# Kernel tuning notes

Hardware: AMD Instinct MI355X
Metric: run time of the kernel (lower is better)

The kernel has to match this reference:

```python
import jax, jax.numpy as jnp
import numpy as np
from jax import lax

B, T, D_IN, D_OUT = 1, 24000, 598, 3
UNITS = [100, 100, 100]
EPS = 0.001


def _lstm(x, W, U, b):
    # x: [B,T,D]; W: [D,4U]; U: [U,4U]; b: [4U]. Keras gate order i,f,g,o.
    units = U.shape[0]
    xW = jnp.einsum('btd,dk->btk', x, W) + b  # precompute input projections

    def step(carry, xw_t):
        h, c = carry
        z = xw_t + h @ U
        i, f, g, o = jnp.split(z, 4, axis=-1)
        c = jax.nn.sigmoid(f) * c + jax.nn.sigmoid(i) * jnp.tanh(g)
        h = jax.nn.sigmoid(o) * jnp.tanh(c)
        return (h, c), h

    h0 = jnp.zeros((x.shape[0], units), x.dtype)
    (_, _), hs = lax.scan(step, (h0, h0), jnp.swapaxes(xW, 0, 1))
    return jnp.swapaxes(hs, 0, 1)  # [B,T,U]


def _bn(x, gamma, beta, mean, var):
    # inference-mode batch norm over last axis
    return (x - mean) * lax.rsqrt(var + EPS) * gamma + beta


def setup_inputs() -> dict:
    key = jax.random.key(0)
    ks = jax.random.split(key, 16)
    out = {"x": jax.random.normal(ks[0], (B, T, D_IN), jnp.float32)}
    d_prev = D_IN
    ki = 1
    for l, u in enumerate(UNITS, start=1):
        out[f"W{l}"] = jax.random.normal(ks[ki], (d_prev, 4 * u), jnp.float32) * (2.0 / d_prev) ** 0.5; ki += 1
        out[f"U{l}"] = jax.random.normal(ks[ki], (u, 4 * u), jnp.float32) * (1.0 / u) ** 0.5; ki += 1
        out[f"b{l}"] = jnp.zeros((4 * u,), jnp.float32)
        out[f"g{l}"] = jnp.ones((u,), jnp.float32)
        out[f"be{l}"] = jnp.zeros((u,), jnp.float32)
        out[f"m{l}"] = jnp.zeros((u,), jnp.float32)
        out[f"v{l}"] = jnp.ones((u,), jnp.float32)
        d_prev = u
    out["Wd"] = jax.random.normal(ks[ki], (d_prev, D_OUT), jnp.float32) * (2.0 / d_prev) ** 0.5
    out["bd"] = jnp.zeros((D_OUT,), jnp.float32)
    return out


def reference(x, W1, U1, b1, g1, be1, m1, v1,
              W2, U2, b2, g2, be2, m2, v2,
              W3, U3, b3, g3, be3, m3, v3, Wd, bd):
    h = x
    params = [(W1, U1, b1, g1, be1, m1, v1),
              (W2, U2, b2, g2, be2, m2, v2),
              (W3, U3, b3, g3, be3, m3, v3)]
    for (W, U, b, g, be, m, v) in params:
        h = _lstm(h, W, U, b)
        h = _bn(h, g, be, m, v)
    return jax.nn.softmax(h @ Wd + bd, axis=-1)
```

## Files before the change

### kernel.cpp

```cpp
#include <hip/hip_runtime.h>

#define T_STEPS 24000
#define DIN 598
#define NU 100
#define NG 400
#define KHALF 52
#define KPAIR 26
#define KPAD 104
#define CHUNK 240
#define NCHUNK 100
#define RING 4
#define RN (RING * CHUNK)

typedef float v2f __attribute__((ext_vector_type(2)));
typedef float v4f __attribute__((ext_vector_type(4)));

#define BARRIER_LDS() asm volatile("s_waitcnt lgkmcnt(0)\n\ts_barrier" ::: "memory")

#define PIN_V2(x) asm volatile("" : "+v"(x))

__device__ __forceinline__ float dpp_add_x1(float x) {
    int y = __builtin_amdgcn_mov_dpp(__float_as_int(x), 0xB1, 0xF, 0xF, true);
    return x + __int_as_float(y);
}

__device__ __forceinline__ void wg_wait_ge(int* flag, int target) {
    if (threadIdx.x == 0) {
        while (__hip_atomic_load(flag, __ATOMIC_RELAXED, __HIP_MEMORY_SCOPE_AGENT) < target)
            __builtin_amdgcn_s_sleep(2);
    }
    __syncthreads();
    __builtin_amdgcn_fence(__ATOMIC_ACQUIRE, "agent");
}
__device__ __forceinline__ void wg_publish(int* a, int va, int* b, int vb) {
    __syncthreads();
    if (threadIdx.x == 0) {
        if (a) __hip_atomic_store(a, va, __ATOMIC_RELEASE, __HIP_MEMORY_SCOPE_AGENT);
        if (b) __hip_atomic_store(b, vb, __ATOMIC_RELEASE, __HIP_MEMORY_SCOPE_AGENT);
    }
}

__device__ __forceinline__ float sigmoid_(float x) {
    return 1.f / (1.f + __expf(-x));
}
__device__ __forceinline__ float tanh_(float x) {
    float e = __expf(2.f * x);
    return 1.f - 2.f / (e + 1.f);
}

__global__ __launch_bounds__(256) void gemm_bias_kernel(
    const float* __restrict__ A, const float* __restrict__ B,
    const float* __restrict__ bias, float* __restrict__ C,
    int M, int N, int K)
{
    __shared__ float As[16][65];
    __shared__ float Bs[16][65];
    const int tid = threadIdx.x;
    const int tx = tid & 15;
    const int ty = tid >> 4;
    const int bm = blockIdx.y * 64;
    const int bn = blockIdx.x * 64;
    float acc[4][4] = {};

    for (int k0 = 0; k0 < K; k0 += 16) {
        #pragma unroll
        for (int p = 0; p < 4; ++p) {
            int e = tid + p * 256;
            int r = e >> 4, cc = e & 15;
            int m = bm + r, k = k0 + cc;
            float v = (m < M && k < K) ? A[(long)m * K + k] : 0.f;
            As[cc][r] = v;
        }
        #pragma unroll
        for (int p = 0; p < 4; ++p) {
            int e = tid + p * 256;
            int r = e >> 6, cc = e & 63;
            int k = k0 + r, n = bn + cc;
            float v = (k < K && n < N) ? B[(long)k * N + n] : 0.f;
            Bs[r][cc] = v;
        }
        __syncthreads();
        #pragma unroll
        for (int kk = 0; kk < 16; ++kk) {
            float a[4], b[4];
            #pragma unroll
            for (int i = 0; i < 4; ++i) a[i] = As[kk][ty * 4 + i];
            #pragma unroll
            for (int j = 0; j < 4; ++j) b[j] = Bs[kk][tx * 4 + j];
            #pragma unroll
            for (int i = 0; i < 4; ++i)
                #pragma unroll
                for (int j = 0; j < 4; ++j)
                    acc[i][j] += a[i] * b[j];
        }
        __syncthreads();
    }
    #pragma unroll
    for (int i = 0; i < 4; ++i) {
        int m = bm + ty * 4 + i;
        if (m >= M) continue;
        #pragma unroll
        for (int j = 0; j < 4; ++j) {
            int n = bn + tx * 4 + j;
            if (n < N) {
                int pn = (n % 100) * 4 + (n / 100);
                C[(long)m * N + pn] = acc[i][j] + bias[n];
            }
        }
    }
}

__device__ void rec_role(
    const float* __restrict__ xz, int xz_ring,
    const float* __restrict__ U,
    float* __restrict__ hout, long h_stride, int h_ring,
    int* flag_up, int* done_self, int* done_down, int* flag_self,
    float* lds)
{
    float* hb0 = lds;
    float* hb1 = lds + KPAD;
    const int tid = threadIdx.x;
    const bool active = tid < 2 * NU;
    const int u = tid >> 1;
    const int s = tid & 1;

    v2f u0[KPAIR], u1[KPAIR], u2[KPAIR], u3[KPAIR];
    if (active) {
        const int k0 = KHALF * s;
        #pragma unroll
        for (int j = 0; j < KPAIR; ++j) {
            int k = k0 + 2 * j;
            float a0 = 0.f, b0 = 0.f, a1 = 0.f, b1 = 0.f,
                  a2 = 0.f, b2 = 0.f, a3 = 0.f, b3 = 0.f;
            if (k < NU) {
                a0 = U[(long)k * NG + u];          a1 = U[(long)k * NG + NU + u];
                a2 = U[(long)k * NG + 2 * NU + u]; a3 = U[(long)k * NG + 3 * NU + u];
            }
            if (k + 1 < NU) {
                b0 = U[(long)(k + 1) * NG + u];          b1 = U[(long)(k + 1) * NG + NU + u];
                b2 = U[(long)(k + 1) * NG + 2 * NU + u]; b3 = U[(long)(k + 1) * NG + 3 * NU + u];
            }
            u0[j] = (v2f){a0, b0}; u1[j] = (v2f){a1, b1};
            u2[j] = (v2f){a2, b2}; u3[j] = (v2f){a3, b3};
            PIN_V2(u0[j]); PIN_V2(u1[j]); PIN_V2(u2[j]); PIN_V2(u3[j]);
        }
    }
    if (tid < KPAD) { hb0[tid] = 0.f; hb1[tid] = 0.f; }
    float c_state = 0.f;
    float2 xwp0 = make_float2(0.f, 0.f), xwp1 = xwp0, xwp2 = xwp0, xwp3 = xwp0;
    float4 hbatch = make_float4(0.f, 0.f, 0.f, 0.f);

    const float* xz_lane = xz + 4 * u + 2 * s;
    float* hout_u = hout + (long)u * h_stride;
    int nxt  = 4 * NG;
    int hoff = 0;
    __syncthreads();

    auto step = [&](const float* hrd, float* hwr, int t) {
        if (active) {
            const v4f* h4 = (const v4f*)(hrd + KHALF * s);
            float2 xw_use = xwp0;
            xwp0 = xwp1; xwp1 = xwp2; xwp2 = xwp3;
            if (t + 4 < T_STEPS) {
                xwp3 = *(const float2*)(xz_lane + nxt);
            }
            nxt += NG;
            if (xz_ring && nxt == RN * NG) nxt = 0;
            v2f a0 = (v2f){0.f, 0.f}, a1 = (v2f){0.f, 0.f};
            v2f a2 = (v2f){0.f, 0.f}, a3 = (v2f){0.f, 0.f};
            #pragma unroll
            for (int q = 0; q < 13; ++q) {
                v4f hv = h4[q];
                v2f plo = hv.xy;
                v2f phi = hv.zw;
                a0 = __builtin_elementwise_fma(u0[2 * q],     plo, a0);
                a1 = __builtin_elementwise_fma(u1[2 * q],     plo, a1);
                a2 = __builtin_elementwise_fma(u2[2 * q],     plo, a2);
                a3 = __builtin_elementwise_fma(u3[2 * q],     plo, a3);
                a0 = __builtin_elementwise_fma(u0[2 * q + 1], phi, a0);
                a1 = __builtin_elementwise_fma(u1[2 * q + 1], phi, a1);
                a2 = __builtin_elementwise_fma(u2[2 * q + 1], phi, a2);
                a3 = __builtin_elementwise_fma(u3[2 * q + 1], phi, a3);
            }
            float ax = a0.x + a0.y;
            float ay = a1.x + a1.y;
            float az = a2.x + a2.y;
            float aw = a3.x + a3.y;
            if (s == 0) { ax += xw_use.x; ay += xw_use.y; }
            else        { az += xw_use.x; aw += xw_use.y; }
            ax = dpp_add_x1(ax);
            ay = dpp_add_x1(ay);
            az = dpp_add_x1(az);
            aw = dpp_add_x1(aw);
            float iv = sigmoid_(ax);
            float fv = sigmoid_(ay);
            float gv = tanh_(az);
            float ov = sigmoid_(aw);
            c_state = fv * c_state + iv * gv;
            float h = ov * tanh_(c_state);
            if (s == 0) {
                hwr[u] = h;
                int ph = t & 3;
                if      (ph == 0) hbatch.x = h;
                else if (ph == 1) hbatch.y = h;
                else if (ph == 2) hbatch.z = h;
                else {
                    hbatch.w = h;
                    *(float4*)(hout_u + hoff) = hbatch;
                    hoff += 4;
                    if (h_ring && hoff == RN) hoff = 0;
                }
            }
        }
        BARRIER_LDS();
    };

    for (int c = 0; c < NCHUNK; ++c) {
        if (flag_up) {
            int tgt = c + 2; if (tgt > NCHUNK) tgt = NCHUNK;
            wg_wait_ge(flag_up, tgt);
        }
        if (done_down && c >= RING) wg_wait_ge(done_down, c - RING + 1);
        if (c == 0 && active) {
            xwp0 = *(const float2*)(xz_lane);
            xwp1 = *(const float2*)(xz_lane + NG);
            xwp2 = *(const float2*)(xz_lane + 2 * NG);
            xwp3 = *(const float2*)(xz_lane + 3 * NG);
        }
        const int t0 = c * CHUNK;
        for (int tt = 0; tt < CHUNK; tt += 2) {
            step(hb0, hb1, t0 + tt);
            step(hb1, hb0, t0 + tt + 1);
        }
        wg_publish(done_self, c + 1, flag_self, c + 1);
    }
}

__device__ void proj_role(
    const float* __restrict__ hin,
    const float* __restrict__ W,
    const float* __restrict__ bias,
    const float* __restrict__ g, const float* __restrict__ be,
    const float* __restrict__ m, const float* __restrict__ v,
    float* __restrict__ xzout,
    int* flag_up, int* done_self, int* done_down, int* flag_self,
    float* lds)
{
    const int tid = threadIdx.x;
    const bool active = tid < 2 * NU;
    const int u = tid >> 1;
    const int s = tid & 1;

    v2f w0[KPAIR], w1[KPAIR], w2[KPAIR], w3[KPAIR];
    float bx = 0.f, by = 0.f;
    if (active) {
        const int k0 = KHALF * s;
        float pbx = 0.f, pby = 0.f, pbz = 0.f, pbw = 0.f;
        #pragma unroll
        for (int j = 0; j < KPAIR; ++j) {
            int k = k0 + 2 * j;
            float a0 = 0.f, b0 = 0.f, a1 = 0.f, b1 = 0.f,
                  a2 = 0.f, b2 = 0.f, a3 = 0.f, b3 = 0.f;
            if (k < NU) {
                float sc = g[k] * rsqrtf(v[k] + 1e-3f);
                float sh = be[k] - m[k] * sc;
                float q0 = W[(long)k * NG + u];
                float q1 = W[(long)k * NG + NU + u];
                float q2 = W[(long)k * NG + 2 * NU + u];
                float q3 = W[(long)k * NG + 3 * NU + u];
                a0 = sc * q0; a1 = sc * q1; a2 = sc * q2; a3 = sc * q3;
                pbx += sh * q0; pby += sh * q1; pbz += sh * q2; pbw += sh * q3;
            }
            if (k + 1 < NU) {
                int kk = k + 1;
                float sc = g[kk] * rsqrtf(v[kk] + 1e-3f);
                float sh = be[kk] - m[kk] * sc;
                float q0 = W[(long)kk * NG + u];
                float q1 = W[(long)kk * NG + NU + u];
                float q2 = W[(long)kk * NG + 2 * NU + u];
                float q3 = W[(long)kk * NG + 3 * NU + u];
                b0 = sc * q0; b1 = sc * q1; b2 = sc * q2; b3 = sc * q3;
                pbx += sh * q0; pby += sh * q1; pbz += sh * q2; pbw += sh * q3;
            }
            w0[j] = (v2f){a0, b0}; w1[j] = (v2f){a1, b1};
            w2[j] = (v2f){a2, b2}; w3[j] = (v2f){a3, b3};
            PIN_V2(w0[j]); PIN_V2(w1[j]); PIN_V2(w2[j]); PIN_V2(w3[j]);
        }
        pbx += __shfl_xor(pbx, 1); pby += __shfl_xor(pby, 1);
        pbz += __shfl_xor(pbz, 1); pbw += __shfl_xor(pbw, 1);
        if (s == 0) { bx = bias[u]          + pbx; by = bias[NU + u]     + pby; }
        else        { bx = bias[2 * NU + u] + pbz; by = bias[3 * NU + u] + pbw; }
    }

    for (int c = 0; c < NCHUNK; ++c) {
        wg_wait_ge(flag_up, c + 1);
        if (c >= RING) wg_wait_ge(done_down, c - RING + 1);
        {
            const int tbase = (c % RING) * CHUNK;
            for (int idx = tid; idx < KPAD * CHUNK; idx += 256) {
                int k = idx / CHUNK, r = idx - k * CHUNK;
                lds[r * KPAD + k] = (k < NU) ? hin[(long)k * RN + tbase + r] : 0.f;
            }
        }
        wg_publish(done_self, c + 1, (int*)0, 0);
        if (active) {
            float* ob = xzout + (size_t)(c % RING) * CHUNK * NG;
            for (int r = 0; r < CHUNK; ++r) {
                const v4f* h4 = (const v4f*)(lds + r * KPAD + KHALF * s);
                v2f a0 = (v2f){0.f, 0.f}, a1 = (v2f){0.f, 0.f};
                v2f a2 = (v2f){0.f, 0.f}, a3 = (v2f){0.f, 0.f};
                #pragma unroll
                for (int q = 0; q < 13; ++q) {
                    v4f hv = h4[q];
                    v2f plo = hv.xy;
                    v2f phi = hv.zw;
                    a0 = __builtin_elementwise_fma(w0[2 * q],     plo, a0);
                    a1 = __builtin_elementwise_fma(w1[2 * q],     plo, a1);
                    a2 = __builtin_elementwise_fma(w2[2 * q],     plo, a2);
                    a3 = __builtin_elementwise_fma(w3[2 * q],     plo, a3);
                    a0 = __builtin_elementwise_fma(w0[2 * q + 1], phi, a0);
                    a1 = __builtin_elementwise_fma(w1[2 * q + 1], phi, a1);
                    a2 = __builtin_elementwise_fma(w2[2 * q + 1], phi, a2);
                    a3 = __builtin_elementwise_fma(w3[2 * q + 1], phi, a3);
                }
                float ax = a0.x + a0.y;
                float ay = a1.x + a1.y;
                float az = a2.x + a2.y;
                float aw = a3.x + a3.y;
                ax = dpp_add_x1(ax);
                ay = dpp_add_x1(ay);
                az = dpp_add_x1(az);
                aw = dpp_add_x1(aw);
                float2 o2 = (s == 0) ? make_float2(ax + bx, ay + by)
                                     : make_float2(az + bx, aw + by);
                *(float2*)&ob[(long)r * NG + 4 * u + 2 * s] = o2;
            }
        }
        wg_publish(flag_self, c + 1, (int*)0, 0);
    }
}

__global__ __launch_bounds__(256)
__attribute__((amdgpu_waves_per_eu(1, 1)))
void lstm_pipe_kernel(
    const float* xw1, const float* U1,
    const float* U2, const float* W2, const float* b2,
    const float* U3, const float* W3, const float* b3,
    const float* g1, const float* be1, const float* m1, const float* v1,
    const float* g2, const float* be2, const float* m2, const float* v2,
    float* h1r, float* h2r, float* xz2r, float* xz3r, float* h3,
    int* f)
{
    extern __shared__ float smem[];
    int* f_h1  = f +   0;
    int* d_p2  = f +  32;
    int* f_xz2 = f +  64;
    int* d_r2  = f +  96;
    int* f_h2  = f + 128;
    int* d_p3  = f + 160;
    int* f_xz3 = f + 192;
    int* d_r3  = f + 224;

    switch (blockIdx.x) {
    case 0: rec_role(xw1, 0, U1, h1r, RN, 1, (int*)0, (int*)0, d_p2, f_h1, smem); break;
    case 1: proj_role(h1r, W2, b2, g1, be1, m1, v1, xz2r, f_h1, d_p2, d_r2, f_xz2, smem); break;
    case 2: rec_role(xz2r, 1, U2, h2r, RN, 1, f_xz2, d_r2, d_p3, f_h2, smem); break;
    case 3: proj_role(h2r, W3, b3, g2, be2, m2, v2, xz3r, f_h2, d_p3, d_r3, f_xz3, smem); break;
    case 4: rec_role(xz3r, 1, U3, h3, T_STEPS, 0, f_xz3, d_r3, (int*)0, (int*)0, smem); break;
    }
}

__global__ __launch_bounds__(256) void dense_softmax_kernel(
    const float* __restrict__ H,
    const float* __restrict__ Wd,
    const float* __restrict__ bd,
    const float* __restrict__ g3, const float* __restrict__ be3,
    const float* __restrict__ m3, const float* __restrict__ v3,
    float* __restrict__ out, int T)
{
    __shared__ float w[300];
    __shared__ float b[3];
    const int tid = threadIdx.x;
    for (int i = tid; i < 300; i += 256) {
        int k = i / 3;
        float sc = g3[k] * rsqrtf(v3[k] + 1e-3f);
        w[i] = Wd[i] * sc;
    }
    if (tid < 3) {
        float acc = bd[tid];
        for (int k = 0; k < NU; ++k) {
            float sc = g3[k] * rsqrtf(v3[k] + 1e-3f);
            float sh = be3[k] - m3[k] * sc;
            acc += sh * Wd[3 * k + tid];
        }
        b[tid] = acc;
    }
    __syncthreads();

    int row = blockIdx.x * blockDim.x + tid;
    if (row >= T) return;
    float s0 = b[0], s1 = b[1], s2 = b[2];
    #pragma unroll 4
    for (int k = 0; k < NU; ++k) {
        float hv = H[(long)k * T + row];
        s0 += hv * w[3 * k + 0];
        s1 += hv * w[3 * k + 1];
        s2 += hv * w[3 * k + 2];
    }
    float mx = fmaxf(s0, fmaxf(s1, s2));
    float e0 = __expf(s0 - mx), e1 = __expf(s1 - mx), e2 = __expf(s2 - mx);
    float inv = 1.f / (e0 + e1 + e2);
    out[(long)row * 3 + 0] = e0 * inv;
    out[(long)row * 3 + 1] = e1 * inv;
    out[(long)row * 3 + 2] = e2 * inv;
}

extern "C" void kernel_launch(void* const* d_in, const int* in_sizes, int n_in,
                              void* d_out, int out_size, void* d_ws, size_t ws_size,
                              hipStream_t stream)
{
    const float* x   = (const float*)d_in[0];
    const float* W1  = (const float*)d_in[1];
    const float* U1  = (const float*)d_in[2];
    const float* b1  = (const float*)d_in[3];
    const float* ga1 = (const float*)d_in[4];
    const float* be1 = (const float*)d_in[5];
    const float* mu1 = (const float*)d_in[6];
    const float* va1 = (const float*)d_in[7];
    const float* W2  = (const float*)d_in[8];
    const float* U2  = (const float*)d_in[9];
    const float* b2  = (const float*)d_in[10];
    const float* ga2 = (const float*)d_in[11];
    const float* be2 = (const float*)d_in[12];
    const float* mu2 = (const float*)d_in[13];
    const float* va2 = (const float*)d_in[14];
    const float* W3  = (const float*)d_in[15];
    const float* U3  = (const float*)d_in[16];
    const float* b3  = (const float*)d_in[17];
    const float* ga3 = (const float*)d_in[18];
    const float* be3 = (const float*)d_in[19];
    const float* mu3 = (const float*)d_in[20];
    const float* va3 = (const float*)d_in[21];
    const float* Wd  = (const float*)d_in[22];
    const float* bd  = (const float*)d_in[23];

    float* xw1  = (float*)d_ws;
    float* h3   = xw1  + (size_t)T_STEPS * NG;
    float* h1r  = h3   + (size_t)T_STEPS * NU;
    float* h2r  = h1r  + (size_t)RN * NU;
    float* xz2r = h2r  + (size_t)RN * NU;
    float* xz3r = xz2r + (size_t)RN * NG;
    int*   flags = (int*)(xz3r + (size_t)RN * NG);
    float* out = (float*)d_out;

    dim3 blk(256);
    dim3 grd((NG + 63) / 64, (T_STEPS + 63) / 64);

    gemm_bias_kernel<<<grd, blk, 0, stream>>>(x, W1, b1, xw1, T_STEPS, NG, DIN);
    hipMemsetAsync(flags, 0, 512 * sizeof(int), stream);
    lstm_pipe_kernel<<<5, 256, CHUNK * KPAD * sizeof(float), stream>>>(
        xw1, U1, U2, W2, b2, U3, W3, b3,
        ga1, be1, mu1, va1, ga2, be2, mu2, va2,
        h1r, h2r, xz2r, xz3r, h3, flags);
    dense_softmax_kernel<<<(T_STEPS + 255) / 256, 256, 0, stream>>>(
        h3, Wd, bd, ga3, be3, mu3, va3, out, T_STEPS);
}
```

Before: 21.07 ms.

## Split LSTM gate work across four lanes per unit with 512-thread blocks

After: 20.43 ms. 1.03x faster.

```diff
diff --git a/kernel.cpp b/kernel.cpp
--- a/kernel.cpp
+++ b/kernel.cpp
@@ -11,6 +11,7 @@
 #define NCHUNK 100
 #define RING 4
 #define RN (RING * CHUNK)
+#define BLK 512
 
 typedef float v2f __attribute__((ext_vector_type(2)));
 typedef float v4f __attribute__((ext_vector_type(4)));
@@ -22,6 +23,10 @@
 __device__ __forceinline__ float dpp_add_x1(float x) {
     int y = __builtin_amdgcn_mov_dpp(__float_as_int(x), 0xB1, 0xF, 0xF, true);
     return x + __int_as_float(y);
+}
+__device__ __forceinline__ float dpp_get_x2(float x) {
+    int y = __builtin_amdgcn_mov_dpp(__float_as_int(x), 0x4E, 0xF, 0xF, true);
+    return __int_as_float(y);
 }
 
 __device__ __forceinline__ void wg_wait_ge(int* flag, int target) {
@@ -120,29 +125,24 @@
     float* hb0 = lds;
     float* hb1 = lds + KPAD;
     const int tid = threadIdx.x;
-    const bool active = tid < 2 * NU;
-    const int u = tid >> 1;
-    const int s = tid & 1;
-
-    v2f u0[KPAIR], u1[KPAIR], u2[KPAIR], u3[KPAIR];
+    const bool active = tid < 4 * NU;
+    const int u  = tid >> 2;
+    const int gp = (tid >> 1) & 1;
+    const int s  = tid & 1;
+
+    v2f wa[KPAIR], wb[KPAIR];
     if (active) {
         const int k0 = KHALF * s;
+        const int ga = 2 * gp * NU, gb = (2 * gp + 1) * NU;
         #pragma unroll
         for (int j = 0; j < KPAIR; ++j) {
             int k = k0 + 2 * j;
-            float a0 = 0.f, b0 = 0.f, a1 = 0.f, b1 = 0.f,
-                  a2 = 0.f, b2 = 0.f, a3 = 0.f, b3 = 0.f;
-            if (k < NU) {
-                a0 = U[(long)k * NG + u];          a1 = U[(long)k * NG + NU + u];
-                a2 = U[(long)k * NG + 2 * NU + u]; a3 = U[(long)k * NG + 3 * NU + u];
-            }
-            if (k + 1 < NU) {
-                b0 = U[(long)(k + 1) * NG + u];          b1 = U[(long)(k + 1) * NG + NU + u];
-                b2 = U[(long)(k + 1) * NG + 2 * NU + u]; b3 = U[(long)(k + 1) * NG + 3 * NU + u];
-            }
-            u0[j] = (v2f){a0, b0}; u1[j] = (v2f){a1, b1};
-            u2[j] = (v2f){a2, b2}; u3[j] = (v2f){a3, b3};
-            PIN_V2(u0[j]); PIN_V2(u1[j]); PIN_V2(u2[j]); PIN_V2(u3[j]);
+            float a0 = 0.f, a1 = 0.f, b0 = 0.f, b1 = 0.f;
+            if (k < NU)     { a0 = U[(long)k * NG + ga + u];       b0 = U[(long)k * NG + gb + u]; }
+            if (k + 1 < NU) { a1 = U[(long)(k + 1) * NG + ga + u]; b1 = U[(long)(k + 1) * NG + gb + u]; }
+            wa[j] = (v2f){a0, a1};
+            wb[j] = (v2f){b0, b1};
+            PIN_V2(wa[j]); PIN_V2(wb[j]);
         }
     }
     if (tid < KPAD) { hb0[tid] = 0.f; hb1[tid] = 0.f; }
@@ -150,7 +150,7 @@
     float2 xwp0 = make_float2(0.f, 0.f), xwp1 = xwp0, xwp2 = xwp0, xwp3 = xwp0;
     float4 hbatch = make_float4(0.f, 0.f, 0.f, 0.f);
 
-    const float* xz_lane = xz + 4 * u + 2 * s;
+    const float* xz_lane = xz + 4 * u + 2 * gp;
     float* hout_u = hout + (long)u * h_stride;
     int nxt  = 4 * NG;
     int hoff = 0;
@@ -159,6 +159,10 @@
     auto step = [&](const float* hrd, float* hwr, int t) {
         if (active) {
             const v4f* h4 = (const v4f*)(hrd + KHALF * s);
+            v4f hbuf[13];
+            #pragma unroll
+            for (int q = 0; q < 13; ++q) hbuf[q] = h4[q];
+            __builtin_amdgcn_sched_barrier(0);
             float2 xw_use = xwp0;
             xwp0 = xwp1; xwp1 = xwp2; xwp2 = xwp3;
             if (t + 4 < T_STEPS) {
@@ -166,39 +170,35 @@
             }
             nxt += NG;
             if (xz_ring && nxt == RN * NG) nxt = 0;
+            __builtin_amdgcn_sched_barrier(0);
             v2f a0 = (v2f){0.f, 0.f}, a1 = (v2f){0.f, 0.f};
-            v2f a2 = (v2f){0.f, 0.f}, a3 = (v2f){0.f, 0.f};
             #pragma unroll
             for (int q = 0; q < 13; ++q) {
-                v4f hv = h4[q];
-                v2f plo = hv.xy;
-                v2f phi = hv.zw;
-                a0 = __builtin_elementwise_fma(u0[2 * q],     plo, a0);
-                a1 = __builtin_elementwise_fma(u1[2 * q],     plo, a1);
-                a2 = __builtin_elementwise_fma(u2[2 * q],     plo, a2);
-                a3 = __builtin_elementwise_fma(u3[2 * q],     plo, a3);
-                a0 = __builtin_elementwise_fma(u0[2 * q + 1], phi, a0);
-                a1 = __builtin_elementwise_fma(u1[2 * q + 1], phi, a1);
-                a2 = __builtin_elementwise_fma(u2[2 * q + 1], phi, a2);
-                a3 = __builtin_elementwise_fma(u3[2 * q + 1], phi, a3);
+                v2f plo = hbuf[q].xy;
+                v2f phi = hbuf[q].zw;
+                a0 = __builtin_elementwise_fma(wa[2 * q],     plo, a0);
+                a1 = __builtin_elementwise_fma(wb[2 * q],     plo, a1);
+                a0 = __builtin_elementwise_fma(wa[2 * q + 1], phi, a0);
+                a1 = __builtin_elementwise_fma(wb[2 * q + 1], phi, a1);
             }
             float ax = a0.x + a0.y;
             float ay = a1.x + a1.y;
-            float az = a2.x + a2.y;
-            float aw = a3.x + a3.y;
-            if (s == 0) { ax += xw_use.x; ay += xw_use.y; }
-            else        { az += xw_use.x; aw += xw_use.y; }
+            if (s == gp) { ax += xw_use.x; ay += xw_use.y; }
             ax = dpp_add_x1(ax);
             ay = dpp_add_x1(ay);
-            az = dpp_add_x1(az);
-            aw = dpp_add_x1(aw);
-            float iv = sigmoid_(ax);
-            float fv = sigmoid_(ay);
-            float gv = tanh_(az);
-            float ov = sigmoid_(aw);
+            float bx2 = dpp_get_x2(ax);
+            float by2 = dpp_get_x2(ay);
+            float zi = gp ? bx2 : ax;
+            float zf = gp ? by2 : ay;
+            float zg = gp ? ax : bx2;
+            float zo = gp ? ay : by2;
+            float iv = sigmoid_(zi);
+            float fv = sigmoid_(zf);
+            float gv = tanh_(zg);
+            float ov = sigmoid_(zo);
             c_state = fv * c_state + iv * gv;
             float h = ov * tanh_(c_state);
-            if (s == 0) {
+            if ((tid & 3) == 0) {
                 hwr[u] = h;
                 int ph = t & 3;
                 if      (ph == 0) hbatch.x = h;
@@ -247,49 +247,45 @@
     float* lds)
 {
     const int tid = threadIdx.x;
-    const bool active = tid < 2 * NU;
-    const int u = tid >> 1;
-    const int s = tid & 1;
-
-    v2f w0[KPAIR], w1[KPAIR], w2[KPAIR], w3[KPAIR];
+    const bool active = tid < 4 * NU;
+    const int u  = tid >> 2;
+    const int gp = (tid >> 1) & 1;
+    const int s  = tid & 1;
+
+    v2f wa[KPAIR], wb[KPAIR];
     float bx = 0.f, by = 0.f;
     if (active) {
         const int k0 = KHALF * s;
-        float pbx = 0.f, pby = 0.f, pbz = 0.f, pbw = 0.f;
+        const int ga = 2 * gp * NU, gb = (2 * gp + 1) * NU;
+        float pba = 0.f, pbb = 0.f;
         #pragma unroll
         for (int j = 0; j < KPAIR; ++j) {
             int k = k0 + 2 * j;
-            float a0 = 0.f, b0 = 0.f, a1 = 0.f, b1 = 0.f,
-                  a2 = 0.f, b2 = 0.f, a3 = 0.f, b3 = 0.f;
+            float a0 = 0.f, a1 = 0.f, b0 = 0.f, b1 = 0.f;
             if (k < NU) {
                 float sc = g[k] * rsqrtf(v[k] + 1e-3f);
                 float sh = be[k] - m[k] * sc;
-                float q0 = W[(long)k * NG + u];
-                float q1 = W[(long)k * NG + NU + u];
-                float q2 = W[(long)k * NG + 2 * NU + u];
-                float q3 = W[(long)k * NG + 3 * NU + u];
-                a0 = sc * q0; a1 = sc * q1; a2 = sc * q2; a3 = sc * q3;
-                pbx += sh * q0; pby += sh * q1; pbz += sh * q2; pbw += sh * q3;
+                float qa = W[(long)k * NG + ga + u];
+                float qb = W[(long)k * NG + gb + u];
+                a0 = sc * qa; b0 = sc * qb;
+                pba += sh * qa; pbb += sh * qb;
             }
             if (k + 1 < NU) {
                 int kk = k + 1;
                 float sc = g[kk] * rsqrtf(v[kk] + 1e-3f);
                 float sh = be[kk] - m[kk] * sc;
-                float q0 = W[(long)kk * NG + u];
-                float q1 = W[(long)kk * NG + NU + u];
-                float q2 = W[(long)kk * NG + 2 * NU + u];
-                float q3 = W[(long)kk * NG + 3 * NU + u];
-                b0 = sc * q0; b1 = sc * q1; b2 = sc * q2; b3 = sc * q3;
-                pbx += sh * q0; pby += sh * q1; pbz += sh * q2; pbw += sh * q3;
-            }
-            w0[j] = (v2f){a0, b0}; w1[j] = (v2f){a1, b1};
-            w2[j] = (v2f){a2, b2}; w3[j] = (v2f){a3, b3};
-            PIN_V2(w0[j]); PIN_V2(w1[j]); PIN_V2(w2[j]); PIN_V2(w3[j]);
-        }
-        pbx += __shfl_xor(pbx, 1); pby += __shfl_xor(pby, 1);
-        pbz += __shfl_xor(pbz, 1); pbw += __shfl_xor(pbw, 1);
-        if (s == 0) { bx = bias[u]          + pbx; by = bias[NU + u]     + pby; }
-        else        { bx = bias[2 * NU + u] + pbz; by = bias[3 * NU + u] + pbw; }
+                float qa = W[(long)kk * NG + ga + u];
+                float qb = W[(long)kk * NG + gb + u];
+                a1 = sc * qa; b1 = sc * qb;
+                pba += sh * qa; pbb += sh * qb;
+            }
+            wa[j] = (v2f){a0, a1};
+            wb[j] = (v2f){b0, b1};
+            PIN_V2(wa[j]); PIN_V2(wb[j]);
+        }
+        pba += __shfl_xor(pba, 1); pbb += __shfl_xor(pbb, 1);
+        bx = bias[ga + u] + pba;
+        by = bias[gb + u] + pbb;
     }
 
     for (int c = 0; c < NCHUNK; ++c) {
@@ -297,7 +293,7 @@
         if (c >= RING) wg_wait_ge(done_down, c - RING + 1);
         {
             const int tbase = (c % RING) * CHUNK;
-            for (int idx = tid; idx < KPAD * CHUNK; idx += 256) {
+            for (int idx = tid; idx < KPAD * CHUNK; idx += BLK) {
                 int k = idx / CHUNK, r = idx - k * CHUNK;
                 lds[r * KPAD + k] = (k < NU) ? hin[(long)k * RN + tbase + r] : 0.f;
             }
@@ -308,40 +304,31 @@
             for (int r = 0; r < CHUNK; ++r) {
                 const v4f* h4 = (const v4f*)(lds + r * KPAD + KHALF * s);
                 v2f a0 = (v2f){0.f, 0.f}, a1 = (v2f){0.f, 0.f};
-                v2f a2 = (v2f){0.f, 0.f}, a3 = (v2f){0.f, 0.f};
                 #pragma unroll
                 for (int q = 0; q < 13; ++q) {
                     v4f hv = h4[q];
                     v2f plo = hv.xy;
                     v2f phi = hv.zw;
-                    a0 = __builtin_elementwise_fma(w0[2 * q],     plo, a0);
-                    a1 = __builtin_elementwise_fma(w1[2 * q],     plo, a1);
-                    a2 = __builtin_elementwise_fma(w2[2 * q],     plo, a2);
-                    a3 = __builtin_elementwise_fma(w3[2 * q],     plo, a3);
-                    a0 = __builtin_elementwise_fma(w0[2 * q + 1], phi, a0);
-                    a1 = __builtin_elementwise_fma(w1[2 * q + 1], phi, a1);
-                    a2 = __builtin_elementwise_fma(w2[2 * q + 1], phi, a2);
-                    a3 = __builtin_elementwise_fma(w3[2 * q + 1], phi, a3);
+                    a0 = __builtin_elementwise_fma(wa[2 * q],     plo, a0);
+                    a1 = __builtin_elementwise_fma(wb[2 * q],     plo, a1);
+                    a0 = __builtin_elementwise_fma(wa[2 * q + 1], phi, a0);
+                    a1 = __builtin_elementwise_fma(wb[2 * q + 1], phi, a1);
                 }
                 float ax = a0.x + a0.y;
                 float ay = a1.x + a1.y;
-                float az = a2.x + a2.y;
-                float aw = a3.x + a3.y;
                 ax = dpp_add_x1(ax);
                 ay = dpp_add_x1(ay);
-                az = dpp_add_x1(az);
-                aw = dpp_add_x1(aw);
-                float2 o2 = (s == 0) ? make_float2(ax + bx, ay + by)
-                                     : make_float2(az + bx, aw + by);
-                *(float2*)&ob[(long)r * NG + 4 * u + 2 * s] = o2;
+                if (s == 0)
+                    *(float2*)&ob[(long)r * NG + 4 * u + 2 * gp]
+                        = make_float2(ax + bx, ay + by);
             }
         }
         wg_publish(flag_self, c + 1, (int*)0, 0);
     }
 }
 
-__global__ __launch_bounds__(256)
-__attribute__((amdgpu_waves_per_eu(1, 1)))
+__global__ __launch_bounds__(BLK)
+__attribute__((amdgpu_waves_per_eu(2, 2)))
 void lstm_pipe_kernel(
     const float* xw1, const float* U1,
     const float* U2, const float* W2, const float* b2,
@@ -458,7 +445,7 @@
 
     gemm_bias_kernel<<<grd, blk, 0, stream>>>(x, W1, b1, xw1, T_STEPS, NG, DIN);
     hipMemsetAsync(flags, 0, 512 * sizeof(int), stream);
-    lstm_pipe_kernel<<<5, 256, CHUNK * KPAD * sizeof(float), stream>>>(
+    lstm_pipe_kernel<<<5, BLK, CHUNK * KPAD * sizeof(float), stream>>>(
         xw1, U1, U2, W2, b2, U3, W3, b3,
         ga1, be1, mu1, va1, ga2, be2, mu2, va2,
         h1r, h2r, xz2r, xz3r, h3, flags);
```
